# Optimization experiments

Measured on AMD Instinct MI355X. Metric: run time of the kernel, lower is better.

Reference implementation:

```python
import jax, jax.numpy as jnp
import numpy as np

EPS = 1e-5
LN_EPS = 1e-5
NUM_EXPERTS = 8
TOP_K = 2
HIDDEN = 1024
INTER = 2048


def _swiglu(x, wg, wu, wd):
    # x: [T,H]; wg,wu: [H,I]; wd: [I,H]
    return (jax.nn.silu(x @ wg) * (x @ wu)) @ wd


def setup_inputs() -> dict:
    key = jax.random.key(0)
    ks = jax.random.split(key, 10)
    B, S, H, I, E = 8, 4096, HIDDEN, INTER, NUM_EXPERTS
    std_h = 1.0 / np.sqrt(H)
    std_i = 1.0 / np.sqrt(I)
    return {
        "x": jax.random.normal(ks[0], (B, S, H), dtype=jnp.float32),
        "ln_scale": jnp.ones((H,), dtype=jnp.float32),
        "ln_bias": jnp.zeros((H,), dtype=jnp.float32),
        "gate_w": jax.random.normal(ks[1], (E, H), dtype=jnp.float32) * 0.01,
        "Wg": jax.random.normal(ks[2], (E, H, I), dtype=jnp.float32) * std_h,
        "Wu": jax.random.normal(ks[3], (E, H, I), dtype=jnp.float32) * std_h,
        "Wd": jax.random.normal(ks[4], (E, I, H), dtype=jnp.float32) * std_i,
        "sWg": jax.random.normal(ks[5], (H, I), dtype=jnp.float32) * std_h,
        "sWu": jax.random.normal(ks[6], (H, I), dtype=jnp.float32) * std_h,
        "sWd": jax.random.normal(ks[7], (I, H), dtype=jnp.float32) * std_i,
    }


def reference(x, ln_scale, ln_bias, gate_w, Wg, Wu, Wd, sWg, sWu, sWd):
    B, S, H = x.shape
    xf = x.reshape(-1, H)  # [T,H]
    # Router: LayerNorm -> gate -> softmax -> top-k -> renormalize
    mu = jnp.mean(xf, axis=-1, keepdims=True)
    var = jnp.var(xf, axis=-1, keepdims=True)
    xn = (xf - mu) * jax.lax.rsqrt(var + LN_EPS) * ln_scale + ln_bias
    logits = xn @ gate_w.T  # [T,E]
    probs = jax.nn.softmax(logits, axis=-1)
    tk_probs, tk_idx = jax.lax.top_k(probs, TOP_K)  # [T,K]
    tk_probs = tk_probs / (jnp.sum(tk_probs, axis=-1, keepdims=True) + EPS)
    # Per-expert combine weight: w[t,e] = sum_k tk_probs[t,k] * (tk_idx[t,k]==e)
    onehot = (tk_idx[..., None] == jnp.arange(NUM_EXPERTS)[None, None, :])  # [T,K,E]
    w = jnp.sum(tk_probs[..., None] * onehot.astype(tk_probs.dtype), axis=1)  # [T,E]
    # Shared expert + weighted routed experts
    out = _swiglu(xf, sWg, sWu, sWd)
    for e in range(NUM_EXPERTS):
        out = out + w[:, e:e + 1] * _swiglu(xf, Wg[e], Wu[e], Wd[e])
    return out.reshape(B, S, H)
```

## Files before the change

kernel.cpp:

```cpp
#include <hip/hip_runtime.h>

#define H 1024
#define ITR 2048
#define NE 8
#define BT 32

typedef __attribute__((ext_vector_type(8))) short short8;
typedef __attribute__((ext_vector_type(4))) float f32x4;

__device__ __forceinline__ float bf2f(unsigned short u){
  union { unsigned int i; float f; } v; v.i = ((unsigned int)u) << 16; return v.f;
}
__device__ __forceinline__ unsigned short f2bf(float f){
  union { unsigned int i; float f; } v; v.f = f;
  unsigned int r = v.i + 0x7FFFu + ((v.i >> 16) & 1u);
  return (unsigned short)(r >> 16);
}
__device__ __forceinline__ void gload16(const void* g, void* l){
  __builtin_amdgcn_global_load_lds((const __attribute__((address_space(1))) void*)g,
                                   (__attribute__((address_space(3))) void*)l, 16, 0, 0);
}

__global__ __launch_bounds__(64) void detect_k(const unsigned int* __restrict__ xw,
                                               int* __restrict__ flag, int* __restrict__ cnt16){
  int lane = threadIdx.x;
  int c = 0;
  #pragma unroll
  for (int i = 0; i < 4; i++){
    unsigned u = xw[lane * 4 + i];
    int e = (u >> 7) & 0xFF;
    c += (e >= 100 && e <= 140) ? 1 : 0;
  }
  #pragma unroll
  for (int off = 32; off; off >>= 1) c += __shfl_xor(c, off);
  if (lane == 0) flag[0] = (c < 128) ? 1 : 0;
  if (lane < 16) cnt16[lane] = 0;
}

__device__ __forceinline__ void loadv16(const void* base, size_t off, int isf, float* out){
  if (isf){
    const float* p = (const float*)base + off;
    float4 a = *(const float4*)p, b = *(const float4*)(p + 4);
    float4 c = *(const float4*)(p + 8), d = *(const float4*)(p + 12);
    out[0]=a.x; out[1]=a.y; out[2]=a.z; out[3]=a.w;
    out[4]=b.x; out[5]=b.y; out[6]=b.z; out[7]=b.w;
    out[8]=c.x; out[9]=c.y; out[10]=c.z; out[11]=c.w;
    out[12]=d.x; out[13]=d.y; out[14]=d.z; out[15]=d.w;
  } else {
    const unsigned short* p = (const unsigned short*)base + off;
    uint4 a = *(const uint4*)p, b = *(const uint4*)(p + 8);
    unsigned short u[16];
    *(uint4*)u = a; *(uint4*)(u + 8) = b;
    #pragma unroll
    for (int j = 0; j < 16; j++) out[j] = bf2f(u[j]);
  }
}

__global__ __launch_bounds__(256) void trans_k(
    const void* __restrict__ rg, const void* __restrict__ ru, const void* __restrict__ rd,
    const void* __restrict__ sg, const void* __restrict__ su, const void* __restrict__ sd,
    unsigned short* __restrict__ arena, const int* __restrict__ flag)
{
  int slot = blockIdx.z / 3, mt = blockIdx.z % 3;
  int e = slot;
  int R = (mt == 2) ? ITR : H;
  int C = (mt == 2) ? H : ITR;
  int c0 = blockIdx.x * 64, r0 = blockIdx.y * 64;
  if (c0 >= C || r0 >= R) return;
  const void* srcv;
  size_t eoff = 0;
  if (e == NE) srcv = (mt == 0) ? sg : ((mt == 1) ? su : sd);
  else { srcv = (mt == 0) ? rg : ((mt == 1) ? ru : rd); eoff = (size_t)e * H * ITR; }
  unsigned short* dst = arena + (size_t)slot * (3u * H * ITR)
                      + (mt == 2 ? (size_t)2 * H * ITR : 0);
  int isf = *flag;
  __shared__ unsigned short tile[64][72];
  int t = threadIdx.x;
  int row = t >> 3, c8 = (t & 7) * 8;
  #pragma unroll
  for (int p = 0; p < 2; p++){
    int r = r0 + row + p * 32;
    unsigned short v[8];
    if (isf){
      const float* s = (const float*)srcv + eoff + (size_t)r * C + c0 + c8;
      float4 a = *(const float4*)s, b = *(const float4*)(s + 4);
      v[0]=f2bf(a.x); v[1]=f2bf(a.y); v[2]=f2bf(a.z); v[3]=f2bf(a.w);
      v[4]=f2bf(b.x); v[5]=f2bf(b.y); v[6]=f2bf(b.z); v[7]=f2bf(b.w);
    } else {
      const unsigned short* s = (const unsigned short*)srcv + eoff + (size_t)r * C + c0 + c8;
      *(uint4*)v = *(const uint4*)s;
    }
    *(uint4*)&tile[row + p * 32][c8] = *(const uint4*)v;
  }
  __syncthreads();
  #pragma unroll
  for (int p = 0; p < 2; p++){
    int c = row + p * 32;
    int dc = c0 + c;
    int dr = (mt == 2) ? dc : (((dc >> 5) << 6) + mt * 32 + (dc & 31));
    unsigned short tmp[8];
    #pragma unroll
    for (int j = 0; j < 8; j++) tmp[j] = tile[c8 + j][c];
    *(uint4*)(dst + (size_t)dr * R + r0 + c8) = *(const uint4*)tmp;
  }
}

__global__ __launch_bounds__(256) void router2_k(
    const void* __restrict__ x, const void* __restrict__ lns, const void* __restrict__ lnb,
    const void* __restrict__ gw, int T, const int* __restrict__ flag,
    int* __restrict__ cnt16, int* __restrict__ lidx, float* __restrict__ lw)
{
  int isf = *flag;
  int tid = threadIdx.x, wv = tid >> 6, lane = tid & 63;
  int t0 = blockIdx.x * BT;
  __shared__ int scc[16], sbase[16];
  __shared__ int sei[2][BT], soi[2][BT];
  __shared__ float swv[2][BT];
  if (tid < 16) scc[tid] = 0;
  float sc[16], bi[16];
  loadv16(lns, (size_t)lane * 16, isf, sc);
  loadv16(lnb, (size_t)lane * 16, isf, bi);
  __syncthreads();

  for (int i = 0; i < BT / 4; i++){
    int tl = i * 4 + wv;
    int tok = t0 + tl;
    if (tok >= T) break;
    float v[16];
    loadv16(x, (size_t)tok * H + lane * 16, isf, v);
    float sum = 0.f, ss = 0.f;
    #pragma unroll
    for (int j = 0; j < 16; j++){ sum += v[j]; ss += v[j] * v[j]; }
    #pragma unroll
    for (int off = 32; off; off >>= 1){ sum += __shfl_xor(sum, off); ss += __shfl_xor(ss, off); }
    float mu = sum * (1.f / H);
    float rstd = rsqrtf(ss * (1.f / H) - mu * mu + 1e-5f);
    float xn[16];
    #pragma unroll
    for (int j = 0; j < 16; j++) xn[j] = (v[j] - mu) * rstd * sc[j] + bi[j];
    float acc[NE];
    #pragma unroll
    for (int e = 0; e < NE; e++){
      float g[16];
      loadv16(gw, (size_t)e * H + lane * 16, isf, g);
      float s = 0.f;
      #pragma unroll
      for (int j = 0; j < 16; j++) s += xn[j] * g[j];
      acc[e] = s;
    }
    #pragma unroll
    for (int off = 32; off; off >>= 1){
      #pragma unroll
      for (int e = 0; e < NE; e++) acc[e] += __shfl_xor(acc[e], off);
    }
    if (lane == 0){
      float m = acc[0];
      #pragma unroll
      for (int e = 1; e < NE; e++) m = fmaxf(m, acc[e]);
      float p[NE], Z = 0.f;
      #pragma unroll
      for (int e = 0; e < NE; e++){ p[e] = expf(acc[e] - m); Z += p[e]; }
      float iZ = 1.f / Z;
      #pragma unroll
      for (int e = 0; e < NE; e++) p[e] *= iZ;
      int i1 = 0;
      #pragma unroll
      for (int e = 1; e < NE; e++) if (p[e] > p[i1]) i1 = e;
      int i2 = (i1 == 0) ? 1 : 0;
      #pragma unroll
      for (int e = 0; e < NE; e++) if (e != i1 && p[e] > p[i2]) i2 = e;
      float s2 = p[i1] + p[i2] + 1e-5f;
      int o1 = atomicAdd(&scc[i1], 1);
      int o2 = atomicAdd(&scc[8 + i2], 1);
      sei[0][tl] = i1; soi[0][tl] = o1; swv[0][tl] = p[i1] / s2;
      sei[1][tl] = i2; soi[1][tl] = o2; swv[1][tl] = p[i2] / s2;
    }
  }
  __syncthreads();
  if (tid < 16) sbase[tid] = atomicAdd(&cnt16[tid], scc[tid]);
  __syncthreads();
  if (tid < 2 * BT){
    int l = tid / BT, t = tid % BT;
    int tok = t0 + t;
    if (tok < T){
      int ctr = l * 8 + sei[l][t];
      int pos = sbase[ctr] + soi[l][t];
      lidx[(size_t)ctr * T + pos] = tok;
      lw[(size_t)ctr * T + pos] = swv[l][t];
    }
  }
}

__global__ __launch_bounds__(64) void scan_k(const int* __restrict__ cnt16,
                                             int* __restrict__ segA, int* __restrict__ segEp,
                                             int* __restrict__ segCnt, int T, int CH,
                                             int L1C, int L2C){
  if (threadIdx.x == 0){
    segA[0] = 0; segEp[0] = T; segCnt[0] = T;
    int b = L1C * CH;
    for (int e = 0; e < 8; e++){
      segA[1 + e] = b; segCnt[1 + e] = cnt16[e];
      b += (cnt16[e] + 255) & ~255;
      segEp[1 + e] = b;
    }
    b = L2C * CH;
    for (int e = 0; e < 8; e++){
      segA[9 + e] = b; segCnt[9 + e] = cnt16[8 + e];
      b += (cnt16[8 + e] + 255) & ~255;
      segEp[9 + e] = b;
    }
  }
}

template<int EPI>
__global__ __launch_bounds__(256, 2) void gemm128_k(
    const void* __restrict__ Asrc, const unsigned short* __restrict__ arena,
    unsigned short* __restrict__ hidden, void* __restrict__ outp,
    const int* __restrict__ segA, const int* __restrict__ segEp, const int* __restrict__ segCnt,
    const int* __restrict__ lidx, const float* __restrict__ lw,
    int T, int CH, int c0chunk, int nh, const int* __restrict__ flag)
{
  constexpr int K  = (EPI == 2) ? ITR : H;
  constexpr int NT = K / 32;

  int tn, tm, chid;
  {
    int P = gridDim.y * gridDim.z;
    int fid = blockIdx.x + gridDim.x * (blockIdx.y + gridDim.y * blockIdx.z);
    if ((P & 7) == 0){
      int xcd = fid & 7;
      int li = fid >> 3;
      int ppx = P >> 3;
      int SS = (EPI == 0) ? 8 : 4;
      if (SS > ppx) SS = ppx;
      int p = li % SS;
      int rest = li / SS;
      tn = rest % (int)gridDim.x;
      int sl = rest / (int)gridDim.x;
      int g = xcd * ppx + sl * SS + p;
      tm = g % (int)gridDim.y;
      chid = c0chunk + g / (int)gridDim.y;
    } else {
      tn = blockIdx.x; tm = blockIdx.y; chid = c0chunk + blockIdx.z;
    }
  }
  int pr0 = chid * CH + tm * 128;

  int s = -1;
  if (pr0 < T) s = 0;
  else {
    #pragma unroll
    for (int i = 1; i <= 16; i++)
      if (pr0 >= segA[i] && pr0 < segEp[i]) s = i;
  }
  if (s < 0) return;
  int cnt = segCnt[s], base = segA[s];
  int slot = (s == 0) ? 8 : ((s - 1) & 7);
  const unsigned short* wT = arena + (size_t)slot * (3u * H * ITR)
                           + (EPI == 2 ? (size_t)2 * H * ITR : 0);
  int isf = *flag;

  __shared__ unsigned short Al[2][128 * 32];
  __shared__ unsigned short Bl[2][128 * 32];

  int tid = threadIdx.x, wid = tid >> 6, l = tid & 63;
  int fr = l & 15, fq = l >> 4;
  int r0l = wid * 32 + (l >> 2);
  int su = (tid & 3) ^ ((l >> 3) & 3);
  size_t hoff = (nh == 2 && (chid & 1)) ? (size_t)CH * ITR : 0;

  const unsigned short* aptr[2];
  const float* afp[2];
  #pragma unroll
  for (int q = 0; q < 2; q++){
    int rloc = r0l + q * 16;
    if (EPI == 2){
      aptr[q] = (const unsigned short*)Asrc + hoff + (size_t)(pr0 - chid * CH + rloc) * ITR + su * 8;
      afp[q] = nullptr;
    } else {
      int rl = pr0 - base + rloc;
      int rc = cnt - 1; rl = rl < rc ? rl : rc;
      int tok = (s == 0) ? rl : lidx[(size_t)(s - 1) * T + rl];
      aptr[q] = (const unsigned short*)Asrc + (size_t)tok * H + su * 8;
      afp[q]  = (const float*)Asrc + (size_t)tok * H + su * 8;
    }
  }
  const unsigned short* bptr[2];
  #pragma unroll
  for (int q = 0; q < 2; q++)
    bptr[q] = wT + (size_t)(tn * 128 + r0l + q * 16) * K + su * 8;

  f32x4 acc[4][4];
  f32x4 zero4 = {0.f, 0.f, 0.f, 0.f};
  #pragma unroll
  for (int m = 0; m < 4; m++)
    #pragma unroll
    for (int n = 0; n < 4; n++) acc[m][n] = zero4;

  int wm = (wid >> 1) * 64, wn = (wid & 1) * 64;

  auto stage = [&](int buf, int kt){
    int k0 = kt * 32;
    #pragma unroll
    for (int q = 0; q < 2; q++){
      int lbyte = (wid * 32 + q * 16) * 64;
      if (EPI == 0 && isf){
        const float* f = afp[q] + k0;
        float4 v0 = *(const float4*)f, v1 = *(const float4*)(f + 4);
        unsigned short w8[8] = {f2bf(v0.x), f2bf(v0.y), f2bf(v0.z), f2bf(v0.w),
                                f2bf(v1.x), f2bf(v1.y), f2bf(v1.z), f2bf(v1.w)};
        *(uint4*)((char*)&Al[buf][0] + (r0l + q * 16) * 64 + (tid & 3) * 16) = *(const uint4*)w8;
      } else {
        gload16(aptr[q] + k0, (char*)&Al[buf][0] + lbyte);
      }
      gload16(bptr[q] + k0, (char*)&Bl[buf][0] + lbyte);
    }
  };

  auto compute = [&](int buf){
    const unsigned short* Ab = &Al[buf][0];
    const unsigned short* Bb = &Bl[buf][0];
    int un = (fq ^ ((fr >> 1) & 3)) * 8;
    __builtin_amdgcn_s_setprio(1);
    short8 a[4], b[4];
    #pragma unroll
    for (int m = 0; m < 4; m++)
      a[m] = *(const short8*)(Ab + (wm + m * 16 + fr) * 32 + un);
    #pragma unroll
    for (int n = 0; n < 4; n++)
      b[n] = *(const short8*)(Bb + (wn + n * 16 + fr) * 32 + un);
    #pragma unroll
    for (int m = 0; m < 4; m++)
      #pragma unroll
      for (int n = 0; n < 4; n++)
        acc[m][n] = __builtin_amdgcn_mfma_f32_16x16x32_bf16(a[m], b[n], acc[m][n], 0, 0, 0);
    __builtin_amdgcn_s_setprio(0);
  };

  stage(0, 0);
  int cur = 0;
  for (int kt = 0; kt < NT; kt++){
    if (kt + 1 < NT) stage(cur ^ 1, kt + 1);
    if (EPI == 0 && isf) asm volatile("s_waitcnt lgkmcnt(0)" ::: "memory");
    if (kt + 1 < NT){
      if (EPI == 0 && isf) asm volatile("s_waitcnt vmcnt(2)" ::: "memory");
      else                 asm volatile("s_waitcnt vmcnt(4)" ::: "memory");
    } else {
      asm volatile("s_waitcnt vmcnt(0)" ::: "memory");
    }
    __builtin_amdgcn_s_barrier();
    compute(cur);
    __builtin_amdgcn_s_barrier();
    cur ^= 1;
  }

  int rb = fq * 4;
  if (EPI == 0){
    int colbase = tn * 64 + (wid & 1) * 32;
    int rl0 = pr0 - chid * CH;
    unsigned short* hb = hidden + hoff;
    #pragma unroll
    for (int m = 0; m < 4; m++){
      #pragma unroll
      for (int j = 0; j < 4; j++){
        int rl = rl0 + wm + m * 16 + rb + j;
        unsigned short* hr = hb + (size_t)rl * ITR + colbase;
        #pragma unroll
        for (int k = 0; k < 2; k++){
          float g = acc[m][k][j], uu = acc[m][k + 2][j];
          hr[k * 16 + fr] = f2bf(g / (1.f + __expf(-g)) * uu);
        }
      }
    }
  } else {
    #pragma unroll
    for (int m = 0; m < 4; m++){
      #pragma unroll
      for (int j = 0; j < 4; j++){
        int pr = pr0 + wm + m * 16 + rb + j;
        int rl = pr - base;
        if (rl < cnt){
          int tok = (s == 0) ? rl : lidx[(size_t)(s - 1) * T + rl];
          size_t ob = (size_t)tok * H + tn * 128 + wn + fr;
          if (s == 0){
            if (isf){
              float* p = (float*)outp + ob;
              #pragma unroll
              for (int n = 0; n < 4; n++) p[n * 16] = acc[m][n][j];
            } else {
              unsigned short* p = (unsigned short*)outp + ob;
              #pragma unroll
              for (int n = 0; n < 4; n++) p[n * 16] = f2bf(acc[m][n][j]);
            }
          } else {
            float wgt = lw[(size_t)(s - 1) * T + rl];
            if (isf){
              float* p = (float*)outp + ob;
              #pragma unroll
              for (int n = 0; n < 4; n++) p[n * 16] += wgt * acc[m][n][j];
            } else {
              unsigned short* p = (unsigned short*)outp + ob;
              #pragma unroll
              for (int n = 0; n < 4; n++) p[n * 16] = f2bf(bf2f(p[n * 16]) + wgt * acc[m][n][j]);
            }
          }
        }
      }
    }
  }
}

extern "C" void kernel_launch(void* const* d_in, const int* in_sizes, int n_in,
                              void* d_out, int out_size, void* d_ws, size_t ws_size,
                              hipStream_t stream)
{
  int T = in_sizes[0] / H;

  char* w = (char*)d_ws;
  auto alloc = [&](size_t b){ char* p = w; w += (b + 255) & ~(size_t)255; return p; };
  int* flag   = (int*)alloc(256);
  int* cnt16  = (int*)alloc(256);
  int* segA   = (int*)alloc(256);
  int* segEp  = (int*)alloc(256);
  int* segCnt = (int*)alloc(256);
  int* lidx   = (int*)alloc((size_t)16 * T * 4);
  float* lw   = (float*)alloc((size_t)16 * T * 4);
  const size_t ARENA = (size_t)9 * 3 * H * ITR * 2;
  unsigned short* arena = (unsigned short*)alloc(ARENA);
  size_t used = (size_t)(w - (char*)d_ws);

  int CH = 2048, nh = 1;
  {
    struct { int ch, n; } lad[4] = {{8192,2},{8192,1},{4096,1},{2048,1}};
    for (int i = 0; i < 4; i++){
      size_t need = used + (size_t)lad[i].n * lad[i].ch * ITR * 2 + 1024;
      if (need <= ws_size){ CH = lad[i].ch; nh = lad[i].n; break; }
    }
  }
  unsigned short* hidden = (unsigned short*)alloc((size_t)nh * CH * ITR * 2);

  int CB1 = (T + CH - 1) / CH;
  int chunks1 = (T + 8 * 255 + CH - 1) / CH;
  int CB2 = CB1 + chunks1;
  int NCHUNK = CB2 + chunks1;

  detect_k<<<1, 64, 0, stream>>>((const unsigned int*)d_in[0], flag, cnt16);
  router2_k<<<(T + BT - 1) / BT, 256, 0, stream>>>(d_in[0], d_in[1], d_in[2], d_in[3],
                                                   T, flag, cnt16, lidx, lw);
  scan_k<<<1, 64, 0, stream>>>(cnt16, segA, segEp, segCnt, T, CH, CB1, CB2);
  trans_k<<<dim3(32, 32, 27), 256, 0, stream>>>(d_in[4], d_in[5], d_in[6],
                                                d_in[7], d_in[8], d_in[9], arena, flag);

  int bnds[4] = {0, CB1, CB2, NCHUNK};
  for (int r = 0; r < 3; r++){
    for (int c = bnds[r]; c < bnds[r + 1]; ){
      int z = (nh == 2 && c + 1 < bnds[r + 1]) ? 2 : 1;
      gemm128_k<0><<<dim3(32, CH / 128, z), 256, 0, stream>>>(
          d_in[0], arena, hidden, nullptr, segA, segEp, segCnt, lidx, lw,
          T, CH, c, nh, flag);
      gemm128_k<2><<<dim3(8, CH / 128, z), 256, 0, stream>>>(
          hidden, arena, hidden, d_out, segA, segEp, segCnt, lidx, lw,
          T, CH, c, nh, flag);
      c += z;
    }
  }
}
```

Baseline: 2.488 ms.

## Merge all chunks of each routing round into single launches when workspace allows

When the workspace can hold a hidden buffer covering every chunk of a round, each of the three rounds (shared, top-1, top-2) is launched as one up-projection and one down-projection kernel across all its chunks, instead of looping over chunks in pairs. Hidden rows are now addressed relative to the round's first chunk, which replaces the old two-half ping-pong offset. The aim is to cut the number of launches and the tail bubbles between small grids, at the cost of a larger hidden buffer. If the workspace is too small it falls back to the old per-chunk loop.

```diff
diff --git a/kernel.cpp b/kernel.cpp
--- a/kernel.cpp
+++ b/kernel.cpp
@@ -218,7 +218,7 @@
     unsigned short* __restrict__ hidden, void* __restrict__ outp,
     const int* __restrict__ segA, const int* __restrict__ segEp, const int* __restrict__ segCnt,
     const int* __restrict__ lidx, const float* __restrict__ lw,
-    int T, int CH, int c0chunk, int nh, const int* __restrict__ flag)
+    int T, int CH, int c0chunk, const int* __restrict__ flag)
 {
   constexpr int K  = (EPI == 2) ? ITR : H;
   constexpr int NT = K / 32;
@@ -267,7 +267,7 @@
   int fr = l & 15, fq = l >> 4;
   int r0l = wid * 32 + (l >> 2);
   int su = (tid & 3) ^ ((l >> 3) & 3);
-  size_t hoff = (nh == 2 && (chid & 1)) ? (size_t)CH * ITR : 0;
+  int hrow0 = pr0 - c0chunk * CH;
 
   const unsigned short* aptr[2];
   const float* afp[2];
@@ -275,7 +275,7 @@
   for (int q = 0; q < 2; q++){
     int rloc = r0l + q * 16;
     if (EPI == 2){
-      aptr[q] = (const unsigned short*)Asrc + hoff + (size_t)(pr0 - chid * CH + rloc) * ITR + su * 8;
+      aptr[q] = (const unsigned short*)Asrc + (size_t)(hrow0 + rloc) * ITR + su * 8;
       afp[q] = nullptr;
     } else {
       int rl = pr0 - base + rloc;
@@ -357,14 +357,12 @@
   int rb = fq * 4;
   if (EPI == 0){
     int colbase = tn * 64 + (wid & 1) * 32;
-    int rl0 = pr0 - chid * CH;
-    unsigned short* hb = hidden + hoff;
     #pragma unroll
     for (int m = 0; m < 4; m++){
       #pragma unroll
       for (int j = 0; j < 4; j++){
-        int rl = rl0 + wm + m * 16 + rb + j;
-        unsigned short* hr = hb + (size_t)rl * ITR + colbase;
+        int rl = hrow0 + wm + m * 16 + rb + j;
+        unsigned short* hr = hidden + (size_t)rl * ITR + colbase;
         #pragma unroll
         for (int k = 0; k < 2; k++){
           float g = acc[m][k][j], uu = acc[m][k + 2][j];
@@ -429,15 +427,24 @@
   unsigned short* arena = (unsigned short*)alloc(ARENA);
   size_t used = (size_t)(w - (char*)d_ws);
 
-  int CH = 2048, nh = 1;
+  int CH = 2048, merged = 0, nh = 1, hidch = 1;
   {
-    struct { int ch, n; } lad[4] = {{8192,2},{8192,1},{4096,1},{2048,1}};
-    for (int i = 0; i < 4; i++){
-      size_t need = used + (size_t)lad[i].n * lad[i].ch * ITR * 2 + 1024;
-      if (need <= ws_size){ CH = lad[i].ch; nh = lad[i].n; break; }
-    }
-  }
-  unsigned short* hidden = (unsigned short*)alloc((size_t)nh * CH * ITR * 2);
+    int mch[3] = {8192, 4096, 2048};
+    for (int i = 0; i < 3 && !merged; i++){
+      int ch = mch[i];
+      int c1 = (T + 8 * 255 + ch - 1) / ch;
+      size_t need = used + (size_t)c1 * ch * ITR * 2 + 1024;
+      if (need <= ws_size){ merged = 1; CH = ch; hidch = c1; }
+    }
+    if (!merged){
+      struct { int ch, n; } lad[4] = {{8192,2},{8192,1},{4096,1},{2048,1}};
+      for (int i = 0; i < 4; i++){
+        size_t need = used + (size_t)lad[i].n * lad[i].ch * ITR * 2 + 1024;
+        if (need <= ws_size){ CH = lad[i].ch; nh = lad[i].n; hidch = lad[i].n; break; }
+      }
+    }
+  }
+  unsigned short* hidden = (unsigned short*)alloc((size_t)hidch * CH * ITR * 2);
 
   int CB1 = (T + CH - 1) / CH;
   int chunks1 = (T + 8 * 255 + CH - 1) / CH;
@@ -452,16 +459,28 @@
                                                 d_in[7], d_in[8], d_in[9], arena, flag);
 
   int bnds[4] = {0, CB1, CB2, NCHUNK};
-  for (int r = 0; r < 3; r++){
-    for (int c = bnds[r]; c < bnds[r + 1]; ){
-      int z = (nh == 2 && c + 1 < bnds[r + 1]) ? 2 : 1;
-      gemm128_k<0><<<dim3(32, CH / 128, z), 256, 0, stream>>>(
+  if (merged){
+    for (int r = 0; r < 3; r++){
+      int ng = bnds[r + 1] - bnds[r];
+      gemm128_k<0><<<dim3(32, CH / 128, ng), 256, 0, stream>>>(
           d_in[0], arena, hidden, nullptr, segA, segEp, segCnt, lidx, lw,
-          T, CH, c, nh, flag);
-      gemm128_k<2><<<dim3(8, CH / 128, z), 256, 0, stream>>>(
+          T, CH, bnds[r], flag);
+      gemm128_k<2><<<dim3(8, CH / 128, ng), 256, 0, stream>>>(
           hidden, arena, hidden, d_out, segA, segEp, segCnt, lidx, lw,
-          T, CH, c, nh, flag);
-      c += z;
-    }
-  }
-}
+          T, CH, bnds[r], flag);
+    }
+  } else {
+    for (int r = 0; r < 3; r++){
+      for (int c = bnds[r]; c < bnds[r + 1]; ){
+        int z = (nh == 2 && c + 1 < bnds[r + 1]) ? 2 : 1;
+        gemm128_k<0><<<dim3(32, CH / 128, z), 256, 0, stream>>>(
+            d_in[0], arena, hidden, nullptr, segA, segEp, segCnt, lidx, lw,
+            T, CH, c, flag);
+        gemm128_k<2><<<dim3(8, CH / 128, z), 256, 0, stream>>>(
+            hidden, arena, hidden, d_out, segA, segEp, segCnt, lidx, lw,
+            T, CH, c, flag);
+        c += z;
+      }
+    }
+  }
+}
```

Result: no change. 2.477 ms (-0.5%).
